# Performance work log

Hardware: AMD Instinct MI355X
Metric: run time of the kernel (lower is better)

## Reference

```python
import jax, jax.numpy as jnp
import numpy as np

H = 12        # num_heads
HD = 64       # head_dim
D = H * HD    # hidden_size = 768
N = 4096      # number of patches (64x64 grid)
SCALE = HD ** -0.5


def _rotate_half(x):
    half = x.shape[-1] // 2
    x1, x2 = x[..., :half], x[..., half:]
    return jnp.concatenate([-x2, x1], axis=-1)


def setup_inputs() -> dict:
    key = jax.random.key(0)
    ks = jax.random.split(key, 7)
    return {
        "hidden_states": jax.random.normal(ks[0], (N, D), jnp.float32),
        "cos": jax.random.uniform(ks[1], (N, HD), jnp.float32),
        "sin": jax.random.uniform(ks[2], (N, HD), jnp.float32),
        "qkv_w": jax.random.normal(ks[3], (D, 3 * D), jnp.float32) * (D ** -0.5),
        "qkv_b": jax.random.normal(ks[4], (3 * D,), jnp.float32) * 0.02,
        "proj_w": jax.random.normal(ks[5], (D, D), jnp.float32) * (D ** -0.5),
        "proj_b": jax.random.normal(ks[6], (D,), jnp.float32) * 0.02,
    }


def reference(hidden_states, cos, sin, qkv_w, qkv_b, proj_w, proj_b):
    n = hidden_states.shape[0]
    # fused QKV projection: (N, 3D) -> (N, 3, H, HD)
    qkv = (hidden_states @ qkv_w + qkv_b).reshape(n, 3, H, HD)
    q, k, v = qkv[:, 0], qkv[:, 1], qkv[:, 2]  # each (N, H, HD)

    # 2-D RoPE (HF apply_rotary_pos_emb_vision): cos/sin broadcast over heads
    c = cos[:, None, :]
    s = sin[:, None, :]
    q = q * c + _rotate_half(q) * s
    k = k * c + _rotate_half(k) * s

    # full bidirectional attention, heads-first layout
    q = q.transpose(1, 0, 2) * SCALE  # (H, N, HD)
    k = k.transpose(1, 0, 2)
    v = v.transpose(1, 0, 2)
    attn = jnp.einsum('hnd,hmd->hnm', q, k)      # (H, N, N)
    attn = jax.nn.softmax(attn, axis=-1)
    out = jnp.einsum('hnm,hmd->hnd', attn, v)    # (H, N, HD)
    out = out.transpose(1, 0, 2).reshape(n, D)
    return out @ proj_w + proj_b
```

## Files before the change

kernel.cpp:

```cpp
#include <hip/hip_runtime.h>
#include <stdint.h>

#define NTOK 4096
#define NH 12
#define HDIM 64
#define DMODEL 768
#define D3 2304

typedef __attribute__((ext_vector_type(8))) __bf16 bf16x8;
typedef __attribute__((ext_vector_type(4))) float f32x4;
typedef __attribute__((ext_vector_type(4))) unsigned int u32x4;

#define MFMA(a, b, c) __builtin_amdgcn_mfma_f32_16x16x32_bf16((a), (b), (c), 0, 0, 0)

__device__ __forceinline__ uint16_t f2bf(float f) {
  uint32_t u = __builtin_bit_cast(uint32_t, f) + 0x8000u;
  return (uint16_t)(u >> 16);
}
__device__ __forceinline__ uint32_t packrd(float a, float b) {
  uint32_t ua = __builtin_bit_cast(uint32_t, a) + 0x8000u;
  uint32_t ub = __builtin_bit_cast(uint32_t, b) + 0x8000u;
  return __builtin_amdgcn_perm(ub, ua, 0x07060302u);
}
__device__ __forceinline__ uint32_t packtr(float a, float b) {
  return __builtin_amdgcn_perm(__builtin_bit_cast(uint32_t, b), __builtin_bit_cast(uint32_t, a),
                               0x07060302u);
}
__device__ __forceinline__ float bf2f(uint16_t u) {
  uint32_t v = ((uint32_t)u) << 16;
  return __builtin_bit_cast(float, v);
}
__device__ __forceinline__ void gld_lds16(const uint16_t* g, uint16_t* l) {
  __builtin_amdgcn_global_load_lds((const __attribute__((address_space(1))) void*)g,
                                   (__attribute__((address_space(3))) void*)l, 16, 0, 0);
}

__global__ void va_cast_bf16(const float* __restrict__ in, uint16_t* __restrict__ out, int n4) {
  int i = blockIdx.x * 256 + threadIdx.x;
  if (i >= n4) return;
  float4 v = ((const float4*)in)[i];
  ((uint2*)out)[i] = make_uint2(packrd(v.x, v.y), packrd(v.z, v.w));
}

__global__ void va_transpose_cast(const float* __restrict__ W, uint16_t* __restrict__ Wt,
                                  int K, int Ncols) {
  __shared__ uint16_t tile[32][36];
  const int t = threadIdx.x;
  const int k0 = blockIdx.y * 32, n0 = blockIdx.x * 32;
  {
    int i = t >> 3, j = (t & 7) * 4;
    float4 v = *(const float4*)(W + (size_t)(k0 + i) * Ncols + n0 + j);
    tile[i][j + 0] = f2bf(v.x);
    tile[i][j + 1] = f2bf(v.y);
    tile[i][j + 2] = f2bf(v.z);
    tile[i][j + 3] = f2bf(v.w);
  }
  __syncthreads();
  {
    int c = t >> 3, kk = (t & 7) * 4;
    uint32_t lo = (uint32_t)tile[kk + 0][c] | ((uint32_t)tile[kk + 1][c] << 16);
    uint32_t hi = (uint32_t)tile[kk + 2][c] | ((uint32_t)tile[kk + 3][c] << 16);
    *(uint2*)(Wt + (size_t)(n0 + c) * K + k0 + kk) = make_uint2(lo, hi);
  }
}

__global__ __launch_bounds__(256) void va_gemm_qkv(const uint16_t* __restrict__ A,
                                                   const uint16_t* __restrict__ Bt,
                                                   const float* __restrict__ bias,
                                                   const float* __restrict__ cosb,
                                                   const float* __restrict__ sinb,
                                                   uint16_t* __restrict__ Qg,
                                                   uint16_t* __restrict__ Kg,
                                                   uint16_t* __restrict__ Vtg) {
  __shared__ uint16_t As[128 * 32];
  __shared__ uint16_t Bs[128 * 32];
  const int t = threadIdx.x;
  const int w = t >> 6, ln = t & 63, quad = ln >> 4, l15 = ln & 15;
  const int m0 = blockIdx.y * 128, n0 = blockIdx.x * 128;
  const int wm = (w & 1) * 64, wn = (w >> 1) * 64;
  const int srow = t >> 2, scol = (t & 3) * 8;
  f32x4 acc[4][4] = {};
  for (int kk = 0; kk < DMODEL; kk += 32) {
#pragma unroll
    for (int p = 0; p < 2; ++p) {
      gld_lds16(A + (size_t)(m0 + p * 64 + srow) * DMODEL + kk + scol,
                As + (p * 64 + w * 16) * 32);
      gld_lds16(Bt + (size_t)(n0 + p * 64 + srow) * DMODEL + kk + scol,
                Bs + (p * 64 + w * 16) * 32);
    }
    __syncthreads();
    bf16x8 af[4], bfr[4];
#pragma unroll
    for (int i = 0; i < 4; ++i) {
      af[i] = *(const bf16x8*)(As + (wm + i * 16 + l15) * 32 + quad * 8);
      bfr[i] = *(const bf16x8*)(Bs + (wn + i * 16 + l15) * 32 + quad * 8);
    }
#pragma unroll
    for (int i = 0; i < 4; ++i)
#pragma unroll
      for (int j = 0; j < 4; ++j) acc[i][j] = MFMA(af[i], bfr[j], acc[i][j]);
    __syncthreads();
  }
  const int col0 = n0 + wn;
  const int type = col0 / DMODEL;
  const int h = (col0 % DMODEL) / HDIM;
  if (type < 2) {
    const float sc = (type == 0) ? (0.125f * 1.4426950408889634f) : 1.0f;
    uint16_t* dst = (type == 0 ? Qg : Kg) + (size_t)h * NTOK * HDIM;
#pragma unroll
    for (int j = 0; j < 2; ++j) {
      const int d = j * 16 + l15, dhi = d + 32;
      const float blo = bias[col0 + d], bhi = bias[col0 + dhi];
#pragma unroll
      for (int i = 0; i < 4; ++i) {
        const int row0 = m0 + wm + i * 16 + quad * 4;
#pragma unroll
        for (int rg = 0; rg < 4; ++rg) {
          const int n = row0 + rg;
          const float a = acc[i][j][rg] + blo;
          const float b = acc[i][j + 2][rg] + bhi;
          const float cl = cosb[(size_t)n * HDIM + d], sl = sinb[(size_t)n * HDIM + d];
          const float ch = cosb[(size_t)n * HDIM + dhi], sh = sinb[(size_t)n * HDIM + dhi];
          dst[(size_t)n * HDIM + d] = f2bf((a * cl - b * sl) * sc);
          dst[(size_t)n * HDIM + dhi] = f2bf((b * ch + a * sh) * sc);
        }
      }
    }
  } else {
    const int win = (m0 + wm) >> 6;
#pragma unroll
    for (int i = 0; i < 4; ++i) {
      const int H = i & 1, hb = (i >> 1) & 1;
      const int colp = win * 32 + quad * 8 + hb * 4;
#pragma unroll
      for (int j = 0; j < 4; ++j) {
        const int d = j * 16 + l15;
        const float bb = bias[col0 + d];
        uint32_t u0 = packrd(acc[i][j][0] + bb, acc[i][j][1] + bb);
        uint32_t u1 = packrd(acc[i][j][2] + bb, acc[i][j][3] + bb);
        *(uint2*)(Vtg + (((size_t)H * NH + h) * HDIM + d) * 2048 + colp) = make_uint2(u0, u1);
      }
    }
  }
}

__global__ __launch_bounds__(256) void va_gemm_proj(const uint16_t* __restrict__ A,
                                                    const uint16_t* __restrict__ Bt,
                                                    const float* __restrict__ bias,
                                                    float* __restrict__ C, int M, int Nc, int K) {
  __shared__ uint16_t As[64 * 32];
  __shared__ uint16_t Bs[128 * 32];
  const int t = threadIdx.x;
  const int w = t >> 6, ln = t & 63, quad = ln >> 4, l15 = ln & 15;
  const int m0 = blockIdx.y * 64, n0 = blockIdx.x * 128;
  const int wn = w * 32;
  const int srow = t >> 2, scol = (t & 3) * 8;
  f32x4 acc[4][2] = {};
  for (int kk = 0; kk < K; kk += 32) {
    if (srow < 64)
      gld_lds16(A + (size_t)(m0 + srow) * K + kk + scol, As + w * 16 * 32);
#pragma unroll
    for (int p = 0; p < 2; ++p)
      gld_lds16(Bt + (size_t)(n0 + p * 64 + srow) * K + kk + scol, Bs + (p * 64 + w * 16) * 32);
    __syncthreads();
    bf16x8 af[4], bfr[2];
#pragma unroll
    for (int i = 0; i < 4; ++i) af[i] = *(const bf16x8*)(As + (i * 16 + l15) * 32 + quad * 8);
#pragma unroll
    for (int j = 0; j < 2; ++j)
      bfr[j] = *(const bf16x8*)(Bs + (wn + j * 16 + l15) * 32 + quad * 8);
#pragma unroll
    for (int i = 0; i < 4; ++i)
#pragma unroll
      for (int j = 0; j < 2; ++j) acc[i][j] = MFMA(af[i], bfr[j], acc[i][j]);
    __syncthreads();
  }
#pragma unroll
  for (int i = 0; i < 4; ++i) {
    int row = m0 + i * 16 + quad * 4;
#pragma unroll
    for (int j = 0; j < 2; ++j) {
      int col = n0 + wn + j * 16 + l15;
      float b = bias[col];
#pragma unroll
      for (int rg = 0; rg < 4; ++rg) C[(size_t)(row + rg) * Nc + col] = acc[i][j][rg] + b;
    }
  }
}

__global__ __launch_bounds__(256, 3) void va_flash10(const uint16_t* __restrict__ Qg,
                                                     const uint16_t* __restrict__ Kg,
                                                     const uint16_t* __restrict__ Vtg,
                                                     uint16_t* __restrict__ Opb,
                                                     float* __restrict__ Lp) {
  __shared__ uint16_t Ks[2][2][64 * 32];
  __shared__ uint16_t Vs[2][2][64 * 32];
  const int t = threadIdx.x;
  const int w = t >> 6, ln = t & 63, quad = ln >> 4, l15 = ln & 15;
  const int h = blockIdx.y;
  const int qb = blockIdx.x & 31, ks = blockIdx.x >> 5;
  const int q0 = qb * 128, key0 = ks * 2048;

  bf16x8 qf[2][2];
#pragma unroll
  for (int s = 0; s < 2; ++s)
#pragma unroll
    for (int c = 0; c < 2; ++c)
      qf[s][c] = *(const bf16x8*)(Qg + ((size_t)h * NTOK + q0 + w * 32 + s * 16 + l15) * HDIM +
                                  c * 32 + quad * 8);
  const u32x4 onesu = {0x3F803F80u, 0x3F803F80u, 0x3F803F80u, 0x3F803F80u};
  const bf16x8 vones = __builtin_bit_cast(bf16x8, onesu);
  f32x4 o[2][4] = {};
  f32x4 ol[2] = {};
  const uint16_t* Kst =
      Kg + ((size_t)h * NTOK + key0 + w * 16 + (ln >> 2)) * HDIM + (ln & 3) * 8;
  const uint16_t* Vst0 =
      Vtg + (((size_t)0 * NH + h) * HDIM + w * 16 + (ln >> 2)) * 2048 + ks * 1024 + (ln & 3) * 8;
  const uint16_t* Vst1 =
      Vtg + (((size_t)1 * NH + h) * HDIM + w * 16 + (ln >> 2)) * 2048 + ks * 1024 + (ln & 3) * 8;

  gld_lds16(Kst, &Ks[0][0][w * 16 * 32]);
  gld_lds16(Kst + 32, &Ks[0][1][w * 16 * 32]);
  gld_lds16(Vst0, &Vs[0][0][w * 16 * 32]);
  gld_lds16(Vst1, &Vs[0][1][w * 16 * 32]);

  for (int kt = 0; kt < 32; ++kt) {
    __syncthreads();
    const int cur = kt & 1;
    if (kt < 31) {
      Kst += 64 * HDIM;
      Vst0 += 32;
      Vst1 += 32;
      gld_lds16(Kst, &Ks[cur ^ 1][0][w * 16 * 32]);
      gld_lds16(Kst + 32, &Ks[cur ^ 1][1][w * 16 * 32]);
      gld_lds16(Vst0, &Vs[cur ^ 1][0][w * 16 * 32]);
      gld_lds16(Vst1, &Vs[cur ^ 1][1][w * 16 * 32]);
    }
    f32x4 st[2][4];
#pragma unroll
    for (int mt = 0; mt < 4; ++mt) {
      bf16x8 ka0 = *(const bf16x8*)(&Ks[cur][0][(mt * 16 + l15) * 32 + quad * 8]);
      bf16x8 ka1 = *(const bf16x8*)(&Ks[cur][1][(mt * 16 + l15) * 32 + quad * 8]);
#pragma unroll
      for (int s = 0; s < 2; ++s) {
        f32x4 z = {};
        z = MFMA(ka0, qf[s][0], z);
        st[s][mt] = MFMA(ka1, qf[s][1], z);
      }
    }
    bf16x8 vf[4][2];
#pragma unroll
    for (int dt = 0; dt < 4; ++dt)
#pragma unroll
      for (int H = 0; H < 2; ++H)
        vf[dt][H] = *(const bf16x8*)(&Vs[cur][H][(dt * 16 + l15) * 32 + quad * 8]);
#pragma unroll
    for (int s = 0; s < 2; ++s) {
      uint32_t Ppk[4][2];
#pragma unroll
      for (int mt = 0; mt < 4; ++mt) {
        float p0 = __builtin_amdgcn_exp2f(st[s][mt][0]);
        float p1 = __builtin_amdgcn_exp2f(st[s][mt][1]);
        float p2 = __builtin_amdgcn_exp2f(st[s][mt][2]);
        float p3 = __builtin_amdgcn_exp2f(st[s][mt][3]);
        Ppk[mt][0] = packtr(p0, p1);
        Ppk[mt][1] = packtr(p2, p3);
      }
#pragma unroll
      for (int H = 0; H < 2; ++H) {
        u32x4 d = {Ppk[H][0], Ppk[H][1], Ppk[H + 2][0], Ppk[H + 2][1]};
        bf16x8 pf = __builtin_bit_cast(bf16x8, d);
#pragma unroll
        for (int dt = 0; dt < 4; ++dt) o[s][dt] = MFMA(vf[dt][H], pf, o[s][dt]);
        ol[s] = MFMA(vones, pf, ol[s]);
      }
    }
  }
  uint16_t* ob = Opb + ((size_t)(ks * NH + h) * HDIM) * NTOK;
#pragma unroll
  for (int s = 0; s < 2; ++s) {
    int q = q0 + w * 32 + s * 16 + l15;
#pragma unroll
    for (int dt = 0; dt < 4; ++dt)
#pragma unroll
      for (int rg = 0; rg < 4; ++rg)
        ob[(size_t)(dt * 16 + quad * 4 + rg) * NTOK + q] = f2bf(o[s][dt][rg]);
    if (quad == 0) Lp[(size_t)(ks * NH + h) * NTOK + q] = ol[s][0];
  }
}

__global__ __launch_bounds__(256) void va_combine2(const uint16_t* __restrict__ Opb,
                                                   const float* __restrict__ Lp,
                                                   uint16_t* __restrict__ Ob) {
  __shared__ uint16_t T[64][72];
  const int h = blockIdx.y;
  const int n0 = blockIdx.x * 64;
  const int t = threadIdx.x;
  const int lane = t & 63, c = t >> 6;
  const int n = n0 + lane;
  float lsum = Lp[(size_t)h * NTOK + n] + Lp[(size_t)(NH + h) * NTOK + n];
  const float inv = 1.0f / lsum;
#pragma unroll
  for (int j = 0; j < 16; j += 2) {
    int d = c * 16 + j;
    float r0 = 0.f, r1 = 0.f;
#pragma unroll
    for (int s = 0; s < 2; ++s) {
      const uint16_t* p = Opb + ((size_t)(s * NH + h) * HDIM + d) * NTOK + n;
      r0 += bf2f(p[0]);
      r1 += bf2f(p[NTOK]);
    }
    *(uint32_t*)(&T[lane][d]) = packrd(r0 * inv, r1 * inv);
  }
  __syncthreads();
  const int row = t >> 2, ch = t & 3;
  uint4 a = *(const uint4*)(&T[row][ch * 16]);
  uint4 b = *(const uint4*)(&T[row][ch * 16 + 8]);
  uint16_t* dst = Ob + (size_t)(n0 + row) * DMODEL + h * HDIM + ch * 16;
  *(uint4*)dst = a;
  *(uint4*)(dst + 8) = b;
}

extern "C" void kernel_launch(void* const* d_in, const int* in_sizes, int n_in, void* d_out,
                              int out_size, void* d_ws, size_t ws_size, hipStream_t stream) {
  (void)in_sizes; (void)n_in; (void)out_size; (void)ws_size;
  const float* hidden = (const float*)d_in[0];
  const float* cosb = (const float*)d_in[1];
  const float* sinb = (const float*)d_in[2];
  const float* qkv_w = (const float*)d_in[3];
  const float* qkv_b = (const float*)d_in[4];
  const float* proj_w = (const float*)d_in[5];
  const float* proj_b = (const float*)d_in[6];
  float* out = (float*)d_out;

  char* ws = (char*)d_ws;
  size_t off = 0;
  auto alloc = [&](size_t bytes) {
    void* p = ws + off;
    off += (bytes + 255) & ~(size_t)255;
    return p;
  };
  uint16_t* Abf = (uint16_t*)alloc((size_t)NTOK * DMODEL * 2);
  uint16_t* Wqt = (uint16_t*)alloc((size_t)D3 * DMODEL * 2);
  uint16_t* Wpt = (uint16_t*)alloc((size_t)DMODEL * DMODEL * 2);
  uint16_t* Qb = (uint16_t*)alloc((size_t)NH * NTOK * HDIM * 2);
  uint16_t* Kb = (uint16_t*)alloc((size_t)NH * NTOK * HDIM * 2);
  uint16_t* Vtb = (uint16_t*)alloc((size_t)2 * NH * HDIM * 2048 * 2);
  uint16_t* Ob = (uint16_t*)alloc((size_t)NTOK * DMODEL * 2);
  uint16_t* Opb = (uint16_t*)alloc((size_t)2 * NH * HDIM * NTOK * 2);
  float* Lp = (float*)alloc((size_t)2 * NH * NTOK * 4);

  va_cast_bf16<<<(NTOK * DMODEL / 4 + 255) / 256, 256, 0, stream>>>(hidden, Abf,
                                                                    NTOK * DMODEL / 4);
  va_transpose_cast<<<dim3(D3 / 32, DMODEL / 32), 256, 0, stream>>>(qkv_w, Wqt, DMODEL, D3);
  va_transpose_cast<<<dim3(DMODEL / 32, DMODEL / 32), 256, 0, stream>>>(proj_w, Wpt, DMODEL,
                                                                        DMODEL);
  va_gemm_qkv<<<dim3(D3 / 128, NTOK / 128), 256, 0, stream>>>(Abf, Wqt, qkv_b, cosb, sinb, Qb,
                                                              Kb, Vtb);
  va_flash10<<<dim3(64, NH), 256, 0, stream>>>(Qb, Kb, Vtb, Opb, Lp);
  va_combine2<<<dim3(NTOK / 64, NH), 256, 0, stream>>>(Opb, Lp, Ob);
  va_gemm_proj<<<dim3(DMODEL / 128, NTOK / 64), 256, 0, stream>>>(Ob, Wpt, proj_b, out, NTOK,
                                                                  DMODEL, DMODEL);
}
```

Before: 200.2 us.

## Store attention partials token-major and pack Q/K RoPE stores as pairs

The flash kernel now writes its partial outputs in a token-major [split][token][768] layout using packed 8-byte stores, instead of a head-dim-major layout written as scattered 2-byte stores. This lets the combine kernel become a simple vectorized elementwise sum and normalise, with no shared-memory transpose. The QKV epilogue also packs each rotated (d, d+32) pair into one 32-bit store. That permutes the head dimension of Q and K identically, which leaves their dot products unchanged. The aim is to cut uncoalesced global writes and the transpose work in the combine step.

Result: no change. 200.0 us (-0.1%).

```diff
diff --git a/kernel.cpp b/kernel.cpp
--- a/kernel.cpp
+++ b/kernel.cpp
@@ -121,8 +121,8 @@
           const float b = acc[i][j + 2][rg] + bhi;
           const float cl = cosb[(size_t)n * HDIM + d], sl = sinb[(size_t)n * HDIM + d];
           const float ch = cosb[(size_t)n * HDIM + dhi], sh = sinb[(size_t)n * HDIM + dhi];
-          dst[(size_t)n * HDIM + d] = f2bf((a * cl - b * sl) * sc);
-          dst[(size_t)n * HDIM + dhi] = f2bf((b * ch + a * sh) * sc);
+          *(uint32_t*)(dst + (size_t)n * HDIM + 2 * d) =
+              packrd((a * cl - b * sl) * sc, (b * ch + a * sh) * sc);
         }
       }
     }
@@ -188,7 +188,7 @@
   }
 }
 
-__global__ __launch_bounds__(256, 3) void va_flash10(const uint16_t* __restrict__ Qg,
+__global__ __launch_bounds__(256, 3) void va_flash11(const uint16_t* __restrict__ Qg,
                                                      const uint16_t* __restrict__ Kg,
                                                      const uint16_t* __restrict__ Vtg,
                                                      uint16_t* __restrict__ Opb,
@@ -276,49 +276,41 @@
       }
     }
   }
-  uint16_t* ob = Opb + ((size_t)(ks * NH + h) * HDIM) * NTOK;
 #pragma unroll
   for (int s = 0; s < 2; ++s) {
-    int q = q0 + w * 32 + s * 16 + l15;
-#pragma unroll
-    for (int dt = 0; dt < 4; ++dt)
-#pragma unroll
-      for (int rg = 0; rg < 4; ++rg)
-        ob[(size_t)(dt * 16 + quad * 4 + rg) * NTOK + q] = f2bf(o[s][dt][rg]);
+    const int q = q0 + w * 32 + s * 16 + l15;
+    uint16_t* row = Opb + ((size_t)ks * NTOK + q) * DMODEL + h * HDIM + quad * 4;
+#pragma unroll
+    for (int dt = 0; dt < 4; ++dt) {
+      uint32_t u0 = packrd(o[s][dt][0], o[s][dt][1]);
+      uint32_t u1 = packrd(o[s][dt][2], o[s][dt][3]);
+      *(uint2*)(row + dt * 16) = make_uint2(u0, u1);
+    }
     if (quad == 0) Lp[(size_t)(ks * NH + h) * NTOK + q] = ol[s][0];
   }
 }
 
-__global__ __launch_bounds__(256) void va_combine2(const uint16_t* __restrict__ Opb,
-                                                   const float* __restrict__ Lp,
-                                                   uint16_t* __restrict__ Ob) {
-  __shared__ uint16_t T[64][72];
-  const int h = blockIdx.y;
-  const int n0 = blockIdx.x * 64;
-  const int t = threadIdx.x;
-  const int lane = t & 63, c = t >> 6;
-  const int n = n0 + lane;
-  float lsum = Lp[(size_t)h * NTOK + n] + Lp[(size_t)(NH + h) * NTOK + n];
-  const float inv = 1.0f / lsum;
-#pragma unroll
-  for (int j = 0; j < 16; j += 2) {
-    int d = c * 16 + j;
-    float r0 = 0.f, r1 = 0.f;
-#pragma unroll
-    for (int s = 0; s < 2; ++s) {
-      const uint16_t* p = Opb + ((size_t)(s * NH + h) * HDIM + d) * NTOK + n;
-      r0 += bf2f(p[0]);
-      r1 += bf2f(p[NTOK]);
-    }
-    *(uint32_t*)(&T[lane][d]) = packrd(r0 * inv, r1 * inv);
-  }
-  __syncthreads();
-  const int row = t >> 2, ch = t & 3;
-  uint4 a = *(const uint4*)(&T[row][ch * 16]);
-  uint4 b = *(const uint4*)(&T[row][ch * 16 + 8]);
-  uint16_t* dst = Ob + (size_t)(n0 + row) * DMODEL + h * HDIM + ch * 16;
-  *(uint4*)dst = a;
-  *(uint4*)(dst + 8) = b;
+__global__ __launch_bounds__(256) void va_combine2r(const uint16_t* __restrict__ Opb,
+                                                    const float* __restrict__ Lp,
+                                                    uint16_t* __restrict__ Ob) {
+  const int idx = blockIdx.x * 256 + threadIdx.x;
+  const int n = idx / 96, c = idx % 96;
+  const int h = c >> 3;
+  const float inv =
+      1.0f / (Lp[(size_t)h * NTOK + n] + Lp[((size_t)NH + h) * NTOK + n]);
+  const uint16_t* p0 = Opb + (size_t)n * DMODEL + c * 8;
+  const uint16_t* p1 = Opb + ((size_t)NTOK + n) * DMODEL + c * 8;
+  uint16_t a[8], b[8];
+  *(uint4*)a = *(const uint4*)p0;
+  *(uint4*)b = *(const uint4*)p1;
+  uint32_t out[4];
+#pragma unroll
+  for (int j = 0; j < 8; j += 2) {
+    float r0 = (bf2f(a[j]) + bf2f(b[j])) * inv;
+    float r1 = (bf2f(a[j + 1]) + bf2f(b[j + 1])) * inv;
+    out[j >> 1] = packrd(r0, r1);
+  }
+  *(uint4*)(Ob + (size_t)n * DMODEL + c * 8) = *(uint4*)out;
 }
 
 extern "C" void kernel_launch(void* const* d_in, const int* in_sizes, int n_in, void* d_out,
@@ -347,7 +339,7 @@
   uint16_t* Kb = (uint16_t*)alloc((size_t)NH * NTOK * HDIM * 2);
   uint16_t* Vtb = (uint16_t*)alloc((size_t)2 * NH * HDIM * 2048 * 2);
   uint16_t* Ob = (uint16_t*)alloc((size_t)NTOK * DMODEL * 2);
-  uint16_t* Opb = (uint16_t*)alloc((size_t)2 * NH * HDIM * NTOK * 2);
+  uint16_t* Opb = (uint16_t*)alloc((size_t)2 * NTOK * DMODEL * 2);
   float* Lp = (float*)alloc((size_t)2 * NH * NTOK * 4);
 
   va_cast_bf16<<<(NTOK * DMODEL / 4 + 255) / 256, 256, 0, stream>>>(hidden, Abf,
@@ -357,8 +349,8 @@
                                                                         DMODEL);
   va_gemm_qkv<<<dim3(D3 / 128, NTOK / 128), 256, 0, stream>>>(Abf, Wqt, qkv_b, cosb, sinb, Qb,
                                                               Kb, Vtb);
-  va_flash10<<<dim3(64, NH), 256, 0, stream>>>(Qb, Kb, Vtb, Opb, Lp);
-  va_combine2<<<dim3(NTOK / 64, NH), 256, 0, stream>>>(Opb, Lp, Ob);
+  va_flash11<<<dim3(64, NH), 256, 0, stream>>>(Qb, Kb, Vtb, Opb, Lp);
+  va_combine2r<<<(NTOK * DMODEL / 8) / 256, 256, 0, stream>>>(Opb, Lp, Ob);
   va_gemm_proj<<<dim3(DMODEL / 128, NTOK / 64), 256, 0, stream>>>(Ob, Wpt, proj_b, out, NTOK,
                                                                   DMODEL, DMODEL);
 }
```
